# Performance work log

Measured on AMD Instinct MI355X. Metric: run time of the kernel, lower is better.

The kernel has to match this reference:

```python
import jax, jax.numpy as jnp
import numpy as np

N_FFT = 256
HOP = 64
HS = 126  # window hop in STFT frames (hard-coded in original)


def _stft(x):
    # torch.stft(center=True, pad_mode='reflect', window=None -> rectangular,
    # onesided=True, normalized=False). x: [B, N] -> [B, T, F] (time-major,
    # matching the module's permute(0,1,3,2)).
    pad = N_FFT // 2
    xp = jnp.pad(x, ((0, 0), (pad, pad)), mode='reflect')
    T = x.shape[-1] // HOP + 1
    idx = jnp.arange(T)[:, None] * HOP + jnp.arange(N_FFT)[None, :]  # [T, n_fft]
    frames = xp[:, idx]  # [B, T, n_fft]
    return jnp.fft.rfft(frames, axis=-1)  # [B, T, F=129]


def _spec_match(mix, aux):
    mixS = _stft(mix[:, 0, :])  # [B, Tm, F] complex
    auxS = _stft(aux[:, 0, :])  # [B, Ta, F] complex
    B, Tm, F = mixS.shape
    Ta = auxS.shape[1]
    length = (Ta - Tm) // HS
    pad = HS - (Ta - Tm) % HS
    auxS = jnp.pad(auxS, ((0, 0), (0, pad), (0, 0)))
    # All sliding windows at once: [B, W, Tm, F]
    W = length + 2
    widx = jnp.arange(W)[:, None] * HS + jnp.arange(Tm)[None, :]  # [W, Tm]
    wins = auxS[:, widx, :]  # [B, W, Tm, F]
    # Real part of complex cosine similarity, elementwise
    m = mixS[:, None]  # [B, 1, Tm, F]
    sim = (m.real * wins.real + m.imag * wins.imag) / (jnp.abs(m) * jnp.abs(wins))
    flat = sim.reshape(B, W, -1)
    n = flat.shape[-1]
    # torch.median = lower median; torch.median returns NaN if any NaN present
    srt = jnp.sort(flat, axis=-1)
    med = srt[..., (n - 1) // 2]
    med = jnp.where(jnp.isnan(flat).any(-1), -jnp.inf, med)
    best = jnp.argmax(med, axis=1)  # [B], first max like Python max()
    sel = jnp.take_along_axis(wins, best[:, None, None, None], axis=1)  # [B,1,Tm,F]
    return jnp.concatenate([sel.real, sel.imag], axis=1)  # [B, 2, Tm, F]


def setup_inputs() -> dict:
    key = jax.random.key(0)
    k1, k2 = jax.random.split(key)
    mix = jax.random.normal(k1, (8, 1, 65536), dtype=jnp.float32)
    aux = jax.random.normal(k2, (8, 1, 262144), dtype=jnp.float32)
    return {"mix": mix, "aux": aux}


def reference(mix, aux):
    return _spec_match(mix, aux)
```

## Files before the change

### kernel.cpp

```cpp
#include <hip/hip_runtime.h>
#include <math.h>

constexpr int NFFT  = 256;
constexpr int HOP   = 64;
constexpr int NBIN  = 129;
constexpr int NB    = 8;
constexpr int LMIX  = 65536;
constexpr int LAUX  = 262144;
constexpr int TM    = 1025;
constexpr int TA    = 4097;
constexpr int TROWS = 4175;
constexpr int HS    = 126;
constexpr int W     = 26;
constexpr int NJOBS = NB * W;
constexpr int NVAL  = TM * NBIN;
constexpr int NVALB = 132232;
constexpr int KMED  = (NVAL - 1) / 2;
constexpr int CHUNKS = 8;
constexpr int NBA   = 1024;
constexpr int FPB   = 8;
constexpr int MIXBLKS = (TM + FPB - 1) / FPB;
constexpr int AUXBLKS = (TROWS + FPB - 1) / FPB;
constexpr int GFPB  = 8;
constexpr int GBLKS = (TM + GFPB - 1) / GFPB;

constexpr size_t MIXN_OFF  = 0;
constexpr size_t MIXN_BYTES = (size_t)NB * TM * NBIN * sizeof(float2);
constexpr size_t AUXN_OFF  = MIXN_OFF + MIXN_BYTES;
constexpr size_t AUXN_BYTES = (size_t)NB * TROWS * NBIN * sizeof(float2);
constexpr size_t HIST_OFF  = AUXN_OFF + AUXN_BYTES;
constexpr size_t HIST_BYTES = (size_t)NJOBS * CHUNKS * NBA * 4;
constexpr size_t CAND_OFF  = HIST_OFF + HIST_BYTES;
constexpr size_t CAND_BYTES = (size_t)NJOBS * NVAL * 4;
constexpr size_t BYTES_OFF = CAND_OFF + CAND_BYTES;
constexpr size_t BYTES_BYTES = (size_t)NJOBS * NVALB;
constexpr size_t NAN_OFF   = BYTES_OFF + BYTES_BYTES;
constexpr size_t NAN_BYTES = (size_t)NJOBS * CHUNKS * 4;
constexpr size_t NCAND_OFF = NAN_OFF + NAN_BYTES;
constexpr size_t SELBIN_OFF= NCAND_OFF + 832;
constexpr size_t KREM_OFF  = SELBIN_OFF + 832;
constexpr size_t MED_OFF   = KREM_OFF + 832;

constexpr float TWOPI_N = (float)(-2.0 * 3.14159265358979323846 / 256.0);

__device__ __forceinline__ float2 twiddle(int k) {
    float s, c;
    sincosf(TWOPI_N * (float)k, &s, &c);
    return make_float2(c, s);
}

__global__ void stft_all(const float* __restrict__ mix, const float* __restrict__ aux,
                         float2* __restrict__ mixN, float2* __restrict__ auxN,
                         unsigned* __restrict__ ncand)
{
    constexpr int NX = 64 * (FPB - 1) + NFFT;
    __shared__ float  xs[NX];
    __shared__ float2 Yl[FPB][16][16];
    __shared__ float2 tw256[256];
    __shared__ float2 cis16[16];

    const int tid  = threadIdx.x;
    const int wgid = blockIdx.x;
    const int b    = wgid & 7;
    const int t    = wgid >> 3;
    const bool isMix = t < MIXBLKS;
    const int f0 = (isMix ? t : t - MIXBLKS) * FPB;
    const int L       = isMix ? LMIX : LAUX;
    const int Tframes = isMix ? TM : TA;
    const int Trows   = isMix ? TM : TROWS;
    const float* x    = isMix ? mix : aux;
    float2* out       = isMix ? mixN : auxN;

    if (wgid == 0 && tid < NJOBS) ncand[tid] = 0u;

    tw256[tid] = twiddle(tid);
    if (tid < 16) cis16[tid] = twiddle(16 * tid);

    for (int i = tid; i < NX; i += 256) {
        int j = f0 * HOP + i - 128;
        if (j < 0) j = -j;
        if (j >= L) j = 2 * L - 2 - j;
        xs[i] = x[(size_t)b * L + j];
    }
    __syncthreads();

    const int n1 = (tid >> 4) & 15;
    const int r  = tid & 15;
    {
        float reA[FPB], imA[FPB];
        #pragma unroll
        for (int f = 0; f < FPB; ++f) { reA[f] = 0.f; imA[f] = 0.f; }
        int idx = 0;
        #pragma unroll
        for (int n2 = 0; n2 < 16; ++n2) {
            float2 tv = cis16[idx];
            #pragma unroll
            for (int f = 0; f < FPB; ++f) {
                float v = xs[f * HOP + n1 + 16 * n2];
                reA[f] = fmaf(v, tv.x, reA[f]);
                imA[f] = fmaf(v, tv.y, imA[f]);
            }
            idx = (idx + r) & 15;
        }
        #pragma unroll
        for (int f = 0; f < FPB; ++f) Yl[f][n1][r] = make_float2(reA[f], imA[f]);
    }
    __syncthreads();

    const float QNAN = __int_as_float(0x7FC00000);
    auto emit = [&](int fr, int k, float ar, float ai) {
        if (fr >= Trows) return;
        float2 o;
        if (fr < Tframes) {
            float inv = rsqrtf(ar * ar + ai * ai);
            o = make_float2(ar * inv, ai * inv);
        } else {
            o = make_float2(QNAN, QNAN);
        }
        out[((size_t)b * Trows + fr) * NBIN + k] = o;
    };

    #pragma unroll 1
    for (int p = 0; p < 2; ++p) {
        const int jjA = tid + 512 * p;
        const int jjB = jjA + 256;
        const int fA = jjA / NBIN, kA = jjA - fA * NBIN;
        const int fB = jjB / NBIN, kB = jjB - fB * NBIN;
        const float2 dkA = tw256[kA];
        const float2 dkB = tw256[kB];
        float trA = 1.f, tiA = 0.f, arA = 0.f, aiA = 0.f;
        float trB = 1.f, tiB = 0.f, arB = 0.f, aiB = 0.f;
        #pragma unroll
        for (int s = 0; s < 16; ++s) {
            float2 yA = Yl[fA][s][kA & 15];
            float2 yB = Yl[fB][s][kB & 15];
            arA = fmaf(trA, yA.x, arA); arA = fmaf(-tiA, yA.y, arA);
            aiA = fmaf(trA, yA.y, aiA); aiA = fmaf( tiA, yA.x, aiA);
            arB = fmaf(trB, yB.x, arB); arB = fmaf(-tiB, yB.y, arB);
            aiB = fmaf(trB, yB.y, aiB); aiB = fmaf( tiB, yB.x, aiB);
            float nrA = trA * dkA.x - tiA * dkA.y;
            tiA = fmaf(trA, dkA.y, tiA * dkA.x); trA = nrA;
            float nrB = trB * dkB.x - tiB * dkB.y;
            tiB = fmaf(trB, dkB.y, tiB * dkB.x); trB = nrB;
        }
        emit(f0 + fA, kA, arA, aiA);
        emit(f0 + fB, kB, arB, aiB);
    }
    if (tid < FPB * NBIN - 1024) {
        const int jj = 1024 + tid;
        const int f = jj / NBIN, k = jj - f * NBIN;
        const float2 dk = tw256[k];
        float tr = 1.f, ti = 0.f, ar = 0.f, ai = 0.f;
        #pragma unroll
        for (int s = 0; s < 16; ++s) {
            float2 y = Yl[f][s][k & 15];
            ar = fmaf(tr, y.x, ar); ar = fmaf(-ti, y.y, ar);
            ai = fmaf(tr, y.y, ai); ai = fmaf( ti, y.x, ai);
            float nr = tr * dk.x - ti * dk.y;
            ti = fmaf(tr, dk.y, ti * dk.x); tr = nr;
        }
        emit(f0 + f, k, ar, ai);
    }
}

__device__ __forceinline__ unsigned flip_key(float s) {
    unsigned u = __float_as_uint(s);
    return (u & 0x80000000u) ? ~u : (u | 0x80000000u);
}
__device__ __forceinline__ unsigned qbin(float s) {
    if (!(s == s)) return (unsigned)(NBA - 1);
    int bq = (int)floorf(fmaf(s, 512.f, 512.f));
    bq = max(0, min(NBA - 1, bq));
    return (unsigned)bq;
}

template<int PER>
__device__ __forceinline__ void rank_find(const unsigned (&bins)[PER], unsigned target,
                                          unsigned& out_bin, unsigned& out_rem)
{
    __shared__ unsigned wtot[4];
    __shared__ unsigned result[2];
    const int tid  = threadIdx.x;
    const int lane = tid & 63;
    const int wid  = tid >> 6;

    unsigned st = 0;
    #pragma unroll
    for (int i = 0; i < PER; ++i) st += bins[i];

    unsigned inc = st;
    #pragma unroll
    for (int d = 1; d < 64; d <<= 1) {
        unsigned v = __shfl_up(inc, d);
        if (lane >= d) inc += v;
    }
    if (lane == 63) wtot[wid] = inc;
    __syncthreads();

    unsigned wbase = 0;
    for (int wme = 0; wme < wid; ++wme) wbase += wtot[wme];
    unsigned ex = wbase + inc - st;
    if ((ex <= target) && (target < ex + st)) {
        unsigned cum = ex;
        #pragma unroll
        for (int i = 0; i < PER; ++i) {
            if (cum + bins[i] > target) {
                result[0] = (unsigned)(tid * PER + i);
                result[1] = target - cum;
                break;
            }
            cum += bins[i];
        }
    }
    __syncthreads();
    out_bin = result[0];
    out_rem = result[1];
}

__global__ void sim_hist(const float2* __restrict__ mixN, const float2* __restrict__ auxN,
                         unsigned* __restrict__ hist, unsigned char* __restrict__ bytes,
                         unsigned* __restrict__ nanCnt)
{
    constexpr int NCOPY   = 4;
    constexpr int HSTRIDE = NBA + 1;
    __shared__ unsigned lh[NCOPY * HSTRIDE];
    __shared__ unsigned bnan;
    const int tid   = threadIdx.x;
    const int wgid  = blockIdx.x;
    const int b     = wgid & 7;
    const int rest  = wgid >> 3;
    const int w     = rest / CHUNKS;
    const int chunk = rest - w * CHUNKS;
    const int job   = b * W + w;
    unsigned* lhc = lh + ((tid >> 4) & (NCOPY - 1)) * HSTRIDE;

    for (int i = tid; i < NCOPY * HSTRIDE; i += 256) lh[i] = 0;
    if (tid == 0) bnan = 0;
    __syncthreads();

    unsigned localnan = 0;
    const float2* mrow = mixN + (size_t)b * TM * NBIN;
    const float2* arow = auxN + ((size_t)b * TROWS + (size_t)w * HS) * NBIN;
    unsigned char* bj = bytes + (size_t)job * NVALB;

    const int pad = b & 1;
    const int lim = pad + ((NVAL - pad) & ~1);

    for (int i = pad + (chunk * 256 + tid) * 2; i < lim; i += CHUNKS * 512) {
        float4 mv = *reinterpret_cast<const float4*>(mrow + i);
        float4 av = *reinterpret_cast<const float4*>(arow + i);
        float s0 = fmaf(mv.x, av.x, mv.y * av.y);
        float s1 = fmaf(mv.z, av.z, mv.w * av.w);
        if (!(s0 == s0)) localnan++;
        if (!(s1 == s1)) localnan++;
        unsigned b0 = qbin(s0), b1 = qbin(s1);
        atomicAdd(&lhc[b0], 1u);
        atomicAdd(&lhc[b1], 1u);
        bj[i]     = (unsigned char)(b0 >> 2);
        bj[i + 1] = (unsigned char)(b1 >> 2);
    }
    if (chunk == 0 && tid == 0) {
        int ie = pad ? 0 : NVAL - 1;
        float2 m = mrow[ie];
        float2 a = arow[ie];
        float s = fmaf(m.x, a.x, m.y * a.y);
        if (!(s == s)) localnan++;
        unsigned be = qbin(s);
        atomicAdd(&lhc[be], 1u);
        bj[ie] = (unsigned char)(be >> 2);
    }
    if (localnan) atomicAdd(&bnan, localnan);
    __syncthreads();

    unsigned* gh = hist + ((size_t)job * CHUNKS + chunk) * NBA;
    for (int i = tid; i < NBA; i += 256)
        gh[i] = lh[i] + lh[HSTRIDE + i] + lh[2 * HSTRIDE + i] + lh[3 * HSTRIDE + i];
    if (tid == 0) nanCnt[job * CHUNKS + chunk] = bnan;
}

__global__ void scan_bins(const unsigned* __restrict__ hist, unsigned* __restrict__ selbin,
                          unsigned* __restrict__ krem)
{
    constexpr int PER = NBA / 256;
    const int tid  = threadIdx.x;
    const int wgid = blockIdx.x;
    const int job  = (wgid & 7) * W + (wgid >> 3);
    const unsigned* h = hist + (size_t)job * CHUNKS * NBA;

    unsigned bins[PER];
    #pragma unroll
    for (int i = 0; i < PER; ++i) {
        unsigned v = 0;
        int bin = tid * PER + i;
        #pragma unroll
        for (int c = 0; c < CHUNKS; ++c) v += h[(size_t)c * NBA + bin];
        bins[i] = v;
    }
    unsigned sb, rem;
    rank_find<PER>(bins, (unsigned)KMED, sb, rem);
    if (tid == 0) { selbin[job] = sb; krem[job] = rem; }
}

__global__ void sim_compact(const float2* __restrict__ mixN, const float2* __restrict__ auxN,
                            const unsigned char* __restrict__ bytes,
                            const unsigned* __restrict__ selbin, unsigned* __restrict__ cand,
                            unsigned* __restrict__ ncand)
{
    const int tid   = threadIdx.x;
    const int wgid  = blockIdx.x;
    const int b     = wgid & 7;
    const int rest  = wgid >> 3;
    const int w     = rest / CHUNKS;
    const int chunk = rest - w * CHUNKS;
    const int job   = b * W + w;
    const unsigned sb = selbin[job];
    const unsigned long long pat = 0x0101010101010101ULL * (unsigned long long)(sb >> 2);

    unsigned* candj  = cand + (size_t)job * NVAL;
    unsigned* ncandj = ncand + job;
    const float2* mrow = mixN + (size_t)b * TM * NBIN;
    const float2* arow = auxN + ((size_t)b * TROWS + (size_t)w * HS) * NBIN;
    const unsigned long long* bj8 =
        reinterpret_cast<const unsigned long long*>(bytes + (size_t)job * NVALB);

    constexpr int NGRP = NVAL / 8;
    for (int g = chunk * 256 + tid; g < NGRP; g += CHUNKS * 256) {
        unsigned long long v = bj8[g];
        unsigned long long x = v ^ pat;
        unsigned long long z = (x - 0x0101010101010101ULL) & ~x & 0x8080808080808080ULL;
        while (z) {
            int e = g * 8 + ((__ffsll(z) - 1) >> 3);
            z &= z - 1;
            float2 m = mrow[e];
            float2 a = arow[e];
            float s = fmaf(m.x, a.x, m.y * a.y);
            if (qbin(s) == sb) {
                unsigned idx = atomicAdd(ncandj, 1u);
                candj[idx] = flip_key(s);
            }
        }
    }
    if (chunk == 0 && tid == 0) {
        int e = NVAL - 1;
        float2 m = mrow[e];
        float2 a = arow[e];
        float s = fmaf(m.x, a.x, m.y * a.y);
        if (qbin(s) == sb) {
            unsigned idx = atomicAdd(ncandj, 1u);
            candj[idx] = flip_key(s);
        }
    }
}

__global__ void select_kernel(const unsigned* __restrict__ cand, const unsigned* __restrict__ ncand,
                              const unsigned* __restrict__ krem, const unsigned* __restrict__ nanCnt,
                              float* __restrict__ med)
{
    __shared__ unsigned h[2048];
    const int wgid = blockIdx.x;
    const int job  = (wgid & 7) * W + (wgid >> 3);
    const int tid  = threadIdx.x;
    const unsigned* c = cand + (size_t)job * NVAL;
    const unsigned n = ncand[job];
    unsigned pref = 0, tgt = krem[job];

    for (int ph = 0; ph < 3; ++ph) {
        for (int i = tid; i < 2048; i += 256) h[i] = 0;
        __syncthreads();
        for (unsigned i = tid; i < n; i += 256) {
            unsigned k = c[i];
            if (ph == 0) atomicAdd(&h[k >> 21], 1u);
            else if (ph == 1) { if ((k >> 21) == (pref >> 21)) atomicAdd(&h[(k >> 10) & 2047u], 1u); }
            else { if ((k >> 10) == (pref >> 10)) atomicAdd(&h[k & 1023u], 1u); }
        }
        __syncthreads();

        unsigned bins[8];
        #pragma unroll
        for (int i = 0; i < 8; ++i) bins[i] = h[tid * 8 + i];
        unsigned sb, rem;
        rank_find<8>(bins, tgt, sb, rem);

        if (ph == 0)      pref = sb << 21;
        else if (ph == 1) pref |= sb << 10;
        else              pref |= sb;
        tgt = rem;
        __syncthreads();
    }

    if (tid == 0) {
        unsigned nan = 0;
        #pragma unroll
        for (int c2 = 0; c2 < CHUNKS; ++c2) nan += nanCnt[job * CHUNKS + c2];
        unsigned key = pref;
        unsigned u = (key & 0x80000000u) ? (key ^ 0x80000000u) : ~key;
        med[job] = (nan > 0u) ? -INFINITY : __uint_as_float(u);
    }
}

__global__ void gather_stft(const float* __restrict__ x, const float* __restrict__ med,
                            float* __restrict__ out)
{
    constexpr int NX = 64 * (GFPB - 1) + NFFT;
    __shared__ float  xs[NX];
    __shared__ float2 Yl[GFPB][16][16];
    __shared__ float2 tw256[256];
    __shared__ float2 cis16[16];
    __shared__ int sh_best;

    const int tid  = threadIdx.x;
    const int wgid = blockIdx.x;
    const int b    = wgid & 7;
    const int t0   = (wgid >> 3) * GFPB;

    if (tid == 0) {
        float mx = -INFINITY; int bi = 0;
        for (int w = 0; w < W; ++w) {
            float v = med[b * W + w];
            if (v > mx) { mx = v; bi = w; }
        }
        sh_best = bi;
    }
    tw256[tid] = twiddle(tid);
    if (tid < 16) cis16[tid] = twiddle(16 * tid);
    __syncthreads();

    const int fr0 = sh_best * HS + t0;

    for (int i = tid; i < NX; i += 256) {
        int j = fr0 * HOP + i - 128;
        if (j < 0) j = -j;
        if (j >= LAUX) j = 2 * LAUX - 2 - j;
        j = max(0, min(LAUX - 1, j));
        xs[i] = x[(size_t)b * LAUX + j];
    }
    __syncthreads();

    const int n1 = (tid >> 4) & 15;
    const int r  = tid & 15;
    {
        float reA[GFPB], imA[GFPB];
        #pragma unroll
        for (int f = 0; f < GFPB; ++f) { reA[f] = 0.f; imA[f] = 0.f; }
        int idx = 0;
        #pragma unroll
        for (int n2 = 0; n2 < 16; ++n2) {
            float2 tv = cis16[idx];
            #pragma unroll
            for (int f = 0; f < GFPB; ++f) {
                float v = xs[f * HOP + n1 + 16 * n2];
                reA[f] = fmaf(v, tv.x, reA[f]);
                imA[f] = fmaf(v, tv.y, imA[f]);
            }
            idx = (idx + r) & 15;
        }
        #pragma unroll
        for (int f = 0; f < GFPB; ++f) Yl[f][n1][r] = make_float2(reA[f], imA[f]);
    }
    __syncthreads();

    auto dotask = [&](int jj) {
        const int f = jj / NBIN, k = jj - f * NBIN;
        const int tt = t0 + f;
        if (tt >= TM) return;
        float ar = 0.f, ai = 0.f;
        if (fr0 + f < TA) {
            const float2 dk = tw256[k];
            float tr = 1.f, ti = 0.f;
            #pragma unroll
            for (int s = 0; s < 16; ++s) {
                float2 y = Yl[f][s][k & 15];
                ar = fmaf(tr, y.x, ar); ar = fmaf(-ti, y.y, ar);
                ai = fmaf(tr, y.y, ai); ai = fmaf( ti, y.x, ai);
                float nr = tr * dk.x - ti * dk.y;
                ti = fmaf(tr, dk.y, ti * dk.x); tr = nr;
            }
        }
        size_t o = (size_t)tt * NBIN + k;
        out[(size_t)(b * 2 + 0) * NVAL + o] = ar;
        out[(size_t)(b * 2 + 1) * NVAL + o] = ai;
    };
    #pragma unroll 1
    for (int p = 0; p < 2; ++p) {
        dotask(tid + 512 * p);
        dotask(tid + 512 * p + 256);
    }
    if (tid < GFPB * NBIN - 1024) dotask(1024 + tid);
}

extern "C" void kernel_launch(void* const* d_in, const int* in_sizes, int n_in,
                              void* d_out, int out_size, void* d_ws, size_t ws_size,
                              hipStream_t stream)
{
    const float* mix = (const float*)d_in[0];
    const float* aux = (const float*)d_in[1];
    float* out = (float*)d_out;
    char* ws = (char*)d_ws;

    float2*   mixN = (float2*)(ws + MIXN_OFF);
    float2*   auxN = (float2*)(ws + AUXN_OFF);
    unsigned* hist = (unsigned*)(ws + HIST_OFF);
    unsigned* cand = (unsigned*)(ws + CAND_OFF);
    unsigned char* byt = (unsigned char*)(ws + BYTES_OFF);
    unsigned* nanC = (unsigned*)(ws + NAN_OFF);
    unsigned* ncand= (unsigned*)(ws + NCAND_OFF);
    unsigned* selb = (unsigned*)(ws + SELBIN_OFF);
    unsigned* krem = (unsigned*)(ws + KREM_OFF);
    float*    med  = (float*)(ws + MED_OFF);

    stft_all<<<(MIXBLKS + AUXBLKS) * NB, 256, 0, stream>>>(mix, aux, mixN, auxN, ncand);
    sim_hist<<<NJOBS * CHUNKS, 256, 0, stream>>>(mixN, auxN, hist, byt, nanC);
    scan_bins<<<NJOBS, 256, 0, stream>>>(hist, selb, krem);
    sim_compact<<<NJOBS * CHUNKS, 256, 0, stream>>>(mixN, auxN, byt, selb, cand, ncand);
    select_kernel<<<NJOBS, 256, 0, stream>>>(cand, ncand, krem, nanC, med);
    gather_stft<<<GBLKS * NB, 256, 0, stream>>>(aux, med, out);
}
```

Measured before the change: 126.5 us.

## Store STFT phase angles instead of unit complex values to halve similarity traffic

The STFT stage now stores a single phase angle per bin (atan2) instead of a normalized complex pair. The similarity kernels then compute cos(phase difference) rather than a two-term dot product. This halves the bytes the repeated histogram and compaction passes read, which are memory bound across 208 window jobs. The cost is atan2f in the STFT and cosf per element, which adds ALU work and can make the median selection differ slightly through rounding. Exact zero bins are mapped to NaN to keep the original NaN behaviour.

```diff
diff --git a/kernel.cpp b/kernel.cpp
--- a/kernel.cpp
+++ b/kernel.cpp
@@ -24,11 +24,11 @@
 constexpr int GFPB  = 8;
 constexpr int GBLKS = (TM + GFPB - 1) / GFPB;
 
-constexpr size_t MIXN_OFF  = 0;
-constexpr size_t MIXN_BYTES = (size_t)NB * TM * NBIN * sizeof(float2);
-constexpr size_t AUXN_OFF  = MIXN_OFF + MIXN_BYTES;
-constexpr size_t AUXN_BYTES = (size_t)NB * TROWS * NBIN * sizeof(float2);
-constexpr size_t HIST_OFF  = AUXN_OFF + AUXN_BYTES;
+constexpr size_t MIXT_OFF  = 0;
+constexpr size_t MIXT_BYTES = (size_t)NB * TM * NBIN * 4;
+constexpr size_t AUXT_OFF  = MIXT_OFF + MIXT_BYTES;
+constexpr size_t AUXT_BYTES = (size_t)NB * TROWS * NBIN * 4;
+constexpr size_t HIST_OFF  = AUXT_OFF + AUXT_BYTES;
 constexpr size_t HIST_BYTES = (size_t)NJOBS * CHUNKS * NBA * 4;
 constexpr size_t CAND_OFF  = HIST_OFF + HIST_BYTES;
 constexpr size_t CAND_BYTES = (size_t)NJOBS * NVAL * 4;
@@ -50,7 +50,7 @@
 }
 
 __global__ void stft_all(const float* __restrict__ mix, const float* __restrict__ aux,
-                         float2* __restrict__ mixN, float2* __restrict__ auxN,
+                         float* __restrict__ mixT, float* __restrict__ auxT,
                          unsigned* __restrict__ ncand)
 {
     constexpr int NX = 64 * (FPB - 1) + NFFT;
@@ -69,7 +69,7 @@
     const int Tframes = isMix ? TM : TA;
     const int Trows   = isMix ? TM : TROWS;
     const float* x    = isMix ? mix : aux;
-    float2* out       = isMix ? mixN : auxN;
+    float* out        = isMix ? mixT : auxT;
 
     if (wgid == 0 && tid < NJOBS) ncand[tid] = 0u;
 
@@ -110,14 +110,13 @@
     const float QNAN = __int_as_float(0x7FC00000);
     auto emit = [&](int fr, int k, float ar, float ai) {
         if (fr >= Trows) return;
-        float2 o;
+        float th;
         if (fr < Tframes) {
-            float inv = rsqrtf(ar * ar + ai * ai);
-            o = make_float2(ar * inv, ai * inv);
+            th = (ar == 0.f && ai == 0.f) ? QNAN : atan2f(ai, ar);
         } else {
-            o = make_float2(QNAN, QNAN);
-        }
-        out[((size_t)b * Trows + fr) * NBIN + k] = o;
+            th = QNAN;
+        }
+        out[((size_t)b * Trows + fr) * NBIN + k] = th;
     };
 
     #pragma unroll 1
@@ -217,7 +216,7 @@
     out_rem = result[1];
 }
 
-__global__ void sim_hist(const float2* __restrict__ mixN, const float2* __restrict__ auxN,
+__global__ void sim_hist(const float* __restrict__ mixT, const float* __restrict__ auxT,
                          unsigned* __restrict__ hist, unsigned char* __restrict__ bytes,
                          unsigned* __restrict__ nanCnt)
 {
@@ -239,35 +238,41 @@
     __syncthreads();
 
     unsigned localnan = 0;
-    const float2* mrow = mixN + (size_t)b * TM * NBIN;
-    const float2* arow = auxN + ((size_t)b * TROWS + (size_t)w * HS) * NBIN;
+    const float* mrow = mixT + (size_t)b * TM * NBIN;
+    const float* arow = auxT + ((size_t)b * TROWS + (size_t)w * HS) * NBIN;
     unsigned char* bj = bytes + (size_t)job * NVALB;
 
     const int pad = b & 1;
-    const int lim = pad + ((NVAL - pad) & ~1);
-
-    for (int i = pad + (chunk * 256 + tid) * 2; i < lim; i += CHUNKS * 512) {
-        float4 mv = *reinterpret_cast<const float4*>(mrow + i);
-        float4 av = *reinterpret_cast<const float4*>(arow + i);
-        float s0 = fmaf(mv.x, av.x, mv.y * av.y);
-        float s1 = fmaf(mv.z, av.z, mv.w * av.w);
-        if (!(s0 == s0)) localnan++;
-        if (!(s1 == s1)) localnan++;
-        unsigned b0 = qbin(s0), b1 = qbin(s1);
-        atomicAdd(&lhc[b0], 1u);
-        atomicAdd(&lhc[b1], 1u);
-        bj[i]     = (unsigned char)(b0 >> 2);
-        bj[i + 1] = (unsigned char)(b1 >> 2);
+    const int lim = pad + ((NVAL - pad) & ~3);
+
+    for (int i = pad + (chunk * 256 + tid) * 4; i < lim; i += CHUNKS * 1024) {
+        float2 m0 = *reinterpret_cast<const float2*>(mrow + i);
+        float2 m1 = *reinterpret_cast<const float2*>(mrow + i + 2);
+        float2 a0 = *reinterpret_cast<const float2*>(arow + i);
+        float2 a1 = *reinterpret_cast<const float2*>(arow + i + 2);
+        float sv[4];
+        sv[0] = cosf(m0.x - a0.x);
+        sv[1] = cosf(m0.y - a0.y);
+        sv[2] = cosf(m1.x - a1.x);
+        sv[3] = cosf(m1.y - a1.y);
+        #pragma unroll
+        for (int u = 0; u < 4; ++u) {
+            if (!(sv[u] == sv[u])) localnan++;
+            unsigned bq = qbin(sv[u]);
+            atomicAdd(&lhc[bq], 1u);
+            bj[i + u] = (unsigned char)(bq >> 2);
+        }
     }
     if (chunk == 0 && tid == 0) {
-        int ie = pad ? 0 : NVAL - 1;
-        float2 m = mrow[ie];
-        float2 a = arow[ie];
-        float s = fmaf(m.x, a.x, m.y * a.y);
-        if (!(s == s)) localnan++;
-        unsigned be = qbin(s);
-        atomicAdd(&lhc[be], 1u);
-        bj[ie] = (unsigned char)(be >> 2);
+        for (int e = 0; e < NVAL; ++e) {
+            if (e == pad) e = lim;
+            if (e >= NVAL) break;
+            float s = cosf(mrow[e] - arow[e]);
+            if (!(s == s)) localnan++;
+            unsigned bq = qbin(s);
+            atomicAdd(&lhc[bq], 1u);
+            bj[e] = (unsigned char)(bq >> 2);
+        }
     }
     if (localnan) atomicAdd(&bnan, localnan);
     __syncthreads();
@@ -301,7 +306,7 @@
     if (tid == 0) { selbin[job] = sb; krem[job] = rem; }
 }
 
-__global__ void sim_compact(const float2* __restrict__ mixN, const float2* __restrict__ auxN,
+__global__ void sim_compact(const float* __restrict__ mixT, const float* __restrict__ auxT,
                             const unsigned char* __restrict__ bytes,
                             const unsigned* __restrict__ selbin, unsigned* __restrict__ cand,
                             unsigned* __restrict__ ncand)
@@ -318,8 +323,8 @@
 
     unsigned* candj  = cand + (size_t)job * NVAL;
     unsigned* ncandj = ncand + job;
-    const float2* mrow = mixN + (size_t)b * TM * NBIN;
-    const float2* arow = auxN + ((size_t)b * TROWS + (size_t)w * HS) * NBIN;
+    const float* mrow = mixT + (size_t)b * TM * NBIN;
+    const float* arow = auxT + ((size_t)b * TROWS + (size_t)w * HS) * NBIN;
     const unsigned long long* bj8 =
         reinterpret_cast<const unsigned long long*>(bytes + (size_t)job * NVALB);
 
@@ -331,9 +336,7 @@
         while (z) {
             int e = g * 8 + ((__ffsll(z) - 1) >> 3);
             z &= z - 1;
-            float2 m = mrow[e];
-            float2 a = arow[e];
-            float s = fmaf(m.x, a.x, m.y * a.y);
+            float s = cosf(mrow[e] - arow[e]);
             if (qbin(s) == sb) {
                 unsigned idx = atomicAdd(ncandj, 1u);
                 candj[idx] = flip_key(s);
@@ -342,9 +345,7 @@
     }
     if (chunk == 0 && tid == 0) {
         int e = NVAL - 1;
-        float2 m = mrow[e];
-        float2 a = arow[e];
-        float s = fmaf(m.x, a.x, m.y * a.y);
+        float s = cosf(mrow[e] - arow[e]);
         if (qbin(s) == sb) {
             unsigned idx = atomicAdd(ncandj, 1u);
             candj[idx] = flip_key(s);
@@ -497,8 +498,8 @@
     float* out = (float*)d_out;
     char* ws = (char*)d_ws;
 
-    float2*   mixN = (float2*)(ws + MIXN_OFF);
-    float2*   auxN = (float2*)(ws + AUXN_OFF);
+    float*    mixT = (float*)(ws + MIXT_OFF);
+    float*    auxT = (float*)(ws + AUXT_OFF);
     unsigned* hist = (unsigned*)(ws + HIST_OFF);
     unsigned* cand = (unsigned*)(ws + CAND_OFF);
     unsigned char* byt = (unsigned char*)(ws + BYTES_OFF);
@@ -508,10 +509,10 @@
     unsigned* krem = (unsigned*)(ws + KREM_OFF);
     float*    med  = (float*)(ws + MED_OFF);
 
-    stft_all<<<(MIXBLKS + AUXBLKS) * NB, 256, 0, stream>>>(mix, aux, mixN, auxN, ncand);
-    sim_hist<<<NJOBS * CHUNKS, 256, 0, stream>>>(mixN, auxN, hist, byt, nanC);
+    stft_all<<<(MIXBLKS + AUXBLKS) * NB, 256, 0, stream>>>(mix, aux, mixT, auxT, ncand);
+    sim_hist<<<NJOBS * CHUNKS, 256, 0, stream>>>(mixT, auxT, hist, byt, nanC);
     scan_bins<<<NJOBS, 256, 0, stream>>>(hist, selb, krem);
-    sim_compact<<<NJOBS * CHUNKS, 256, 0, stream>>>(mixN, auxN, byt, selb, cand, ncand);
+    sim_compact<<<NJOBS * CHUNKS, 256, 0, stream>>>(mixT, auxT, byt, selb, cand, ncand);
     select_kernel<<<NJOBS, 256, 0, stream>>>(cand, ncand, krem, nanC, med);
     gather_stft<<<GBLKS * NB, 256, 0, stream>>>(aux, med, out);
 }
```

After: 130.2 us. 3.0% more time.
